# Kernel optimization log

Hardware: AMD Instinct MI355X
Metric: run time of the kernel (lower is better)

The kernel has to match this reference:

```python
import jax, jax.numpy as jnp
import numpy as np

N_NODES = 50000
N_EDGES = 600000
IN_C, HID_C, OUT_C = 128, 128, 64
NUM_GRAPHS = 512


def sage_conv(x, src, dst, Wl, bl, Wr):
    """PyG SAGEConv (aggr='mean'): out = mean_{j->i} x_j @ Wl + bl + x_i @ Wr."""
    n = x.shape[0]
    msg = x[src]  # [E, d] gather
    agg = jax.ops.segment_sum(msg, dst, num_segments=n)
    deg = jax.ops.segment_sum(jnp.ones((src.shape[0], 1), x.dtype), dst, num_segments=n)
    agg = agg / jnp.maximum(deg, 1.0)
    return agg @ Wl + bl + x @ Wr


def setup_inputs() -> dict:
    key = jax.random.key(0)
    ks = jax.random.split(key, 12)
    x = jax.random.normal(ks[0], (N_NODES, IN_C), dtype=jnp.float32)
    edge_index = jax.random.randint(ks[1], (2, N_EDGES), 0, N_NODES, dtype=jnp.int32)
    cluster = jnp.sort(jax.random.randint(ks[2], (N_NODES,), 0, NUM_GRAPHS, dtype=jnp.int32))
    def lin(k, din, dout):
        s = 1.0 / np.sqrt(din)
        return (jax.random.uniform(k, (din, dout), jnp.float32, -s, s))
    return {
        "x": x, "edge_index": edge_index, "cluster": cluster,
        "Wl0": lin(ks[3], IN_C, HID_C), "bl0": jnp.zeros((HID_C,), jnp.float32), "Wr0": lin(ks[4], IN_C, HID_C),
        "Wl1": lin(ks[5], HID_C, HID_C), "bl1": jnp.zeros((HID_C,), jnp.float32), "Wr1": lin(ks[6], HID_C, HID_C),
        "Wl2": lin(ks[7], HID_C, OUT_C), "bl2": jnp.zeros((OUT_C,), jnp.float32), "Wr2": lin(ks[8], HID_C, OUT_C),
    }


def reference(x, edge_index, cluster, Wl0, bl0, Wr0, Wl1, bl1, Wr1, Wl2, bl2, Wr2):
    src, dst = edge_index[0], edge_index[1]
    out = None
    # hidden SAGEConv layers + relu (dropout inactive in eval)
    for Wl, bl, Wr in ((Wl0, bl0, Wr0), (Wl1, bl1, Wr1)):
        out = sage_conv(x, src, dst, Wl, bl, Wr)
        x = jax.nn.relu(out)
    # scatter-mean graph pooling over cluster ids
    gsum = jax.ops.segment_sum(x, cluster, num_segments=NUM_GRAPHS)
    gcnt = jax.ops.segment_sum(jnp.ones((x.shape[0], 1), x.dtype), cluster, num_segments=NUM_GRAPHS)
    g = gsum / jnp.maximum(gcnt, 1.0)
    # final conv + log-softmax over classes
    xf = sage_conv(x, src, dst, Wl2, bl2, Wr2)
    return (jax.nn.log_softmax(xf, axis=-1), out, g)
```

## Files before the change

kernel.cpp:

```cpp
#include <hip/hip_runtime.h>
#include <math.h>

#define NN 50000
#define NE 600000
#define NG 512

typedef unsigned int u32;
typedef unsigned short u16;
typedef unsigned char u8;

typedef __attribute__((ext_vector_type(8))) short bf16x8;
typedef __attribute__((ext_vector_type(4))) float f32x4;
typedef __attribute__((ext_vector_type(4))) unsigned int u32x4;

__device__ __forceinline__ float bf2f(u16 u) {
  return __uint_as_float(((u32)u) << 16);
}
__device__ __forceinline__ u16 f2bf(float f) {
  u32 u = __float_as_uint(f);
  u32 lsb = (u >> 16) & 1u;
  u += 0x7fffu + lsb;
  return (u16)(u >> 16);
}

__device__ __forceinline__ u8 f2q(float f) {
  u32 b = __float_as_uint(f);
  u32 s = (b >> 24) & 0x80u;
  u32 mag = b & 0x7fffffffu;
  u32 lsb = (mag >> 20) & 1u;
  mag += 0x7ffffu + lsb;
  int t = (int)(mag >> 20) - 960;
  u32 em = (t < 0) ? 0u : ((t > 0x7e) ? 0x7eu : (u32)t);
  return (u8)(s | em);
}
__device__ __forceinline__ float q2f(u32 u, int k) {
  u32 s8 = (u >> (8 * k)) & 0xffu;
  u32 em = s8 & 0x7fu;
  u32 bits = ((s8 & 0x80u) << 24) | ((em << 20) + 0x3c000000u);
  return em ? __uint_as_float(bits) : 0.f;
}

__global__ __launch_bounds__(256)
void prep_k(const float* __restrict__ x, u32* __restrict__ xb, u16* __restrict__ xq16,
            const int* __restrict__ ei, int* __restrict__ deg,
            const float* __restrict__ Wl0, const float* __restrict__ Wr0, u16* __restrict__ WbT0,
            const float* __restrict__ Wl1, const float* __restrict__ Wr1, u16* __restrict__ WbT1,
            const float* __restrict__ Wl2, u16* __restrict__ WlT2,
            const float* __restrict__ Wr2, u16* __restrict__ WrT2) {
  int b = blockIdx.x;
  int tid = threadIdx.x;
  if (b < 12500) {
    int t = b * 256 + tid;
    float2 v = ((const float2*)x)[t];
    xb[t] = (u32)f2bf(v.x) | ((u32)f2bf(v.y) << 16);
    xq16[t] = (u16)f2q(v.x) | ((u16)f2q(v.y) << 8);
  } else if (b < 14844) {
    int e = (b - 12500) * 256 + tid;
    if (e < NE) atomicAdd(&deg[ei[NE + e]], 1);
  } else if (b < 15100) {
    bool w1 = (b >= 14972);
    int t = (b - (w1 ? 14972 : 14844)) * 256 + tid;
    int n = t >> 8;
    int k = t & 255;
    const float* Wl = w1 ? Wl1 : Wl0;
    const float* Wr = w1 ? Wr1 : Wr0;
    float v = (k < 128) ? Wl[k * 128 + n] : Wr[(k - 128) * 128 + n];
    int c = k >> 3, e = k & 7;
    u16* dst = w1 ? WbT1 : WbT0;
    dst[n * 256 + (((c ^ (n & 7)) << 3) | e)] = f2bf(v);
  } else {
    bool wr = (b >= 15132);
    int t = (b - (wr ? 15132 : 15100)) * 256 + tid;
    int n = t >> 7;
    int k = t & 127;
    const float* W = wr ? Wr2 : Wl2;
    float v = W[k * 64 + n];
    int c = k >> 3, e = k & 7;
    u16* dst = wr ? WrT2 : WlT2;
    dst[n * 128 + (((c ^ (n & 7)) << 3) | e)] = f2bf(v);
  }
}

__global__ __launch_bounds__(256)
void scan1_k(const int* __restrict__ deg, int* __restrict__ bsum) {
  __shared__ int s[256];
  int idx = blockIdx.x * 256 + threadIdx.x;
  int v = (idx < NN) ? deg[idx] : 0;
  s[threadIdx.x] = v;
  __syncthreads();
  for (int off = 128; off > 0; off >>= 1) {
    if (threadIdx.x < off) s[threadIdx.x] += s[threadIdx.x + off];
    __syncthreads();
  }
  if (threadIdx.x == 0) bsum[blockIdx.x] = s[0];
}

__global__ __launch_bounds__(256)
void scan2_k(const int* __restrict__ bsum, int* __restrict__ bofs, int* __restrict__ row_ptr) {
  __shared__ int s[256];
  int t = threadIdx.x;
  int v = (t < 196) ? bsum[t] : 0;
  s[t] = v;
  __syncthreads();
  for (int off = 1; off < 256; off <<= 1) {
    int add = (t >= off) ? s[t - off] : 0;
    __syncthreads();
    s[t] += add;
    __syncthreads();
  }
  if (t < 196) bofs[t] = s[t] - v;
  if (t == 0) row_ptr[NN] = NE;
}

__global__ __launch_bounds__(256)
void scan3_k(const int* __restrict__ deg, const int* __restrict__ bofs,
             int* __restrict__ row_ptr, int* __restrict__ cursor) {
  __shared__ int s[256];
  int idx = blockIdx.x * 256 + threadIdx.x;
  int t = threadIdx.x;
  int v = (idx < NN) ? deg[idx] : 0;
  s[t] = v;
  __syncthreads();
  for (int off = 1; off < 256; off <<= 1) {
    int add = (t >= off) ? s[t - off] : 0;
    __syncthreads();
    s[t] += add;
    __syncthreads();
  }
  if (idx < NN) {
    int p = bofs[blockIdx.x] + s[t] - v;
    row_ptr[idx] = p;
    cursor[idx] = p;
  }
}

__global__ __launch_bounds__(256)
void fill_k(const int* __restrict__ ei, int* __restrict__ cursor, int* __restrict__ perm) {
  int e = blockIdx.x * 256 + threadIdx.x;
  if (e >= NE) return;
  int pos = atomicAdd(&cursor[ei[NE + e]], 1);
  perm[pos] = ei[e];
}

__global__ __launch_bounds__(256)
void gatherq_k(const u8* __restrict__ xq, const int* __restrict__ row_ptr,
               const int* __restrict__ perm, u16* __restrict__ aggb) {
  int wave = threadIdx.x >> 6;
  int lane = threadIdx.x & 63;
  int grp  = lane >> 3;
  int li   = lane & 7;
  int n = (blockIdx.x * 4 + wave) * 8 + grp;
  int ns = min(n, NN - 1);
  int beg = row_ptr[ns];
  int cnt = row_ptr[ns + 1] - beg;
  int beg_s = min(beg, NE - 1);
  int last = max(cnt - 1, 0);
  int m = max(cnt, __shfl_xor(cnt, 8));
  m = max(m, __shfl_xor(m, 16));
  int jmax = max(m, __shfl_xor(m, 32));
  float acc[16];
#pragma unroll
  for (int i = 0; i < 16; i++) acc[i] = 0.f;
  const u32x4* xv = (const u32x4*)xq;
  for (int base = 0; base < jmax; base += 8) {
    int idx[8];
#pragma unroll
    for (int j = 0; j < 8; j++) idx[j] = perm[beg_s + min(base + j, last)];
    u32x4 v[8];
#pragma unroll
    for (int j = 0; j < 8; j++) v[j] = xv[(size_t)idx[j] * 8 + li];
#pragma unroll
    for (int j = 0; j < 8; j++) {
      bool live = (base + j) < cnt;
#pragma unroll
      for (int w = 0; w < 4; w++) {
        u32 u = v[j][w];
#pragma unroll
        for (int k = 0; k < 4; k++) {
          float f = q2f(u, k);
          acc[w * 4 + k] += live ? f : 0.f;
        }
      }
    }
  }
  float inv = 1.0f / fmaxf((float)cnt, 1.0f);
  u32 o[8];
#pragma unroll
  for (int p = 0; p < 8; p++)
    o[p] = (u32)f2bf(acc[2 * p] * inv) | ((u32)f2bf(acc[2 * p + 1] * inv) << 16);
  if (n < NN) {
    u32x4* dst = (u32x4*)(aggb + (size_t)n * 128);
    dst[li * 2]     = (u32x4){o[0], o[1], o[2], o[3]};
    dst[li * 2 + 1] = (u32x4){o[4], o[5], o[6], o[7]};
  }
}

__global__ __launch_bounds__(256)
void gatherq64_k(const u8* __restrict__ yq, const int* __restrict__ row_ptr,
                 const int* __restrict__ perm, u16* __restrict__ aggy) {
  int wave = threadIdx.x >> 6;
  int lane = threadIdx.x & 63;
  int grp  = lane >> 2;
  int li   = lane & 3;
  int n = (blockIdx.x * 4 + wave) * 16 + grp;
  int ns = min(n, NN - 1);
  int beg = row_ptr[ns];
  int cnt = row_ptr[ns + 1] - beg;
  int beg_s = min(beg, NE - 1);
  int last = max(cnt - 1, 0);
  int m = max(cnt, __shfl_xor(cnt, 4));
  m = max(m, __shfl_xor(m, 8));
  m = max(m, __shfl_xor(m, 16));
  int jmax = max(m, __shfl_xor(m, 32));
  float acc[16];
#pragma unroll
  for (int i = 0; i < 16; i++) acc[i] = 0.f;
  const u32x4* xv = (const u32x4*)yq;
  for (int base = 0; base < jmax; base += 8) {
    int idx[8];
#pragma unroll
    for (int j = 0; j < 8; j++) idx[j] = perm[beg_s + min(base + j, last)];
    u32x4 v[8];
#pragma unroll
    for (int j = 0; j < 8; j++) v[j] = xv[(size_t)idx[j] * 4 + li];
#pragma unroll
    for (int j = 0; j < 8; j++) {
      bool live = (base + j) < cnt;
#pragma unroll
      for (int w = 0; w < 4; w++) {
        u32 u = v[j][w];
#pragma unroll
        for (int k = 0; k < 4; k++) {
          float f = q2f(u, k);
          acc[w * 4 + k] += live ? f : 0.f;
        }
      }
    }
  }
  float inv = 1.0f / fmaxf((float)cnt, 1.0f);
  u32 o[8];
#pragma unroll
  for (int p = 0; p < 8; p++)
    o[p] = (u32)f2bf(acc[2 * p] * inv) | ((u32)f2bf(acc[2 * p + 1] * inv) << 16);
  if (n < NN) {
    u32x4* dst = (u32x4*)(aggy + (size_t)n * 64);
    dst[li * 2]     = (u32x4){o[0], o[1], o[2], o[3]};
    dst[li * 2 + 1] = (u32x4){o[4], o[5], o[6], o[7]};
  }
}

template<bool WRITE_PRE, bool WRITE_XQ>
__global__ __launch_bounds__(256)
void sage_mfma_v2_k(const u16* __restrict__ aggb, const u16* __restrict__ xbin,
                    const u16* __restrict__ WbT, const float* __restrict__ bl,
                    u16* __restrict__ xb_out, float* __restrict__ out_pre,
                    u8* __restrict__ xq_out) {
  __shared__ u16 wsh[128 * 256];
  int tid = threadIdx.x;
  {
    const u32x4* g = (const u32x4*)WbT;
    u32x4* l = (u32x4*)wsh;
#pragma unroll
    for (int i = 0; i < 16; i++)
      l[tid + i * 256] = g[tid + i * 256];
  }
  __syncthreads();

  int wave = tid >> 6;
  int lane = tid & 63;
  int quad = lane >> 4;
  int m16  = lane & 15;
  int r0 = blockIdx.x * 64 + wave * 16;

  int rowA = min(r0 + m16, NN - 1);
  const u16* pa = aggb + (size_t)rowA * 128 + quad * 8;
  const u16* px = xbin + (size_t)rowA * 128 + quad * 8;
  bf16x8 a[8];
#pragma unroll
  for (int j = 0; j < 4; j++) a[j]     = *(const bf16x8*)(pa + j * 32);
#pragma unroll
  for (int j = 0; j < 4; j++) a[4 + j] = *(const bf16x8*)(px + j * 32);

  f32x4 acc[8];
#pragma unroll
  for (int nt = 0; nt < 8; nt++) acc[nt] = (f32x4){0.f, 0.f, 0.f, 0.f};

  int swz = m16 & 7;
#pragma unroll
  for (int ks = 0; ks < 8; ks++) {
#pragma unroll
    for (int nt = 0; nt < 8; nt++) {
      const u16* bp = wsh + (nt * 16 + m16) * 256 + (((quad + ks * 4) ^ swz) << 3);
      bf16x8 b = *(const bf16x8*)bp;
      acc[nt] = __builtin_amdgcn_mfma_f32_16x16x32_bf16(a[ks], b, acc[nt], 0, 0, 0);
    }
  }

  float bv[8];
#pragma unroll
  for (int nt = 0; nt < 8; nt++) bv[nt] = bl[nt * 16 + m16];

  int rbase = r0 + quad * 4;
#pragma unroll
  for (int r = 0; r < 4; r++) {
    int row = rbase + r;
    if (row < NN) {
#pragma unroll
      for (int nt = 0; nt < 8; nt++) {
        int col = nt * 16 + m16;
        float v = acc[nt][r] + bv[nt];
        if (WRITE_PRE) out_pre[(size_t)row * 128 + col] = v;
        float rl = fmaxf(v, 0.f);
        xb_out[(size_t)row * 128 + col] = f2bf(rl);
        if (WRITE_XQ) xq_out[(size_t)row * 128 + col] = f2q(rl);
      }
    }
  }
}

__global__ __launch_bounds__(256)
void post_k(const u16* __restrict__ xb2, const int* __restrict__ cluster,
            float* __restrict__ g, const u16* __restrict__ WlT2,
            u8* __restrict__ yq) {
  __shared__ u16 wsh[64 * 128];
  int tid = threadIdx.x;
  if (blockIdx.x < NG) {
    float* sh = (float*)wsh;
    int gid = blockIdx.x;
    int ch = tid & 127;
    int half = tid >> 7;
    int lo = 0, hi = NN;
    while (lo < hi) { int mid = (lo + hi) >> 1; if (cluster[mid] < gid) lo = mid + 1; else hi = mid; }
    int beg = lo;
    hi = NN;
    while (lo < hi) { int mid = (lo + hi) >> 1; if (cluster[mid] < gid + 1) lo = mid + 1; else hi = mid; }
    int end = lo;
    float s0 = 0.f, s1 = 0.f;
    int n = beg + half;
    for (; n + 2 < end; n += 4) {
      s0 += bf2f(xb2[(size_t)n * 128 + ch]);
      s1 += bf2f(xb2[(size_t)(n + 2) * 128 + ch]);
    }
    if (n < end) s0 += bf2f(xb2[(size_t)n * 128 + ch]);
    sh[tid] = s0 + s1;
    __syncthreads();
    if (tid < 128) {
      float s = sh[tid] + sh[tid + 128];
      g[gid * 128 + tid] = s / fmaxf((float)(end - beg), 1.0f);
    }
    return;
  }
  int bid = blockIdx.x - NG;
  {
    const u32x4* gw = (const u32x4*)WlT2;
    u32x4* l = (u32x4*)wsh;
#pragma unroll
    for (int i = 0; i < 4; i++)
      l[tid + i * 256] = gw[tid + i * 256];
  }
  __syncthreads();

  int wave = tid >> 6;
  int lane = tid & 63;
  int quad = lane >> 4;
  int m16  = lane & 15;
  int r0 = bid * 64 + wave * 16;

  int rowA = min(r0 + m16, NN - 1);
  const u16* px = xb2 + (size_t)rowA * 128 + quad * 8;
  bf16x8 a[4];
#pragma unroll
  for (int j = 0; j < 4; j++) a[j] = *(const bf16x8*)(px + j * 32);

  f32x4 acc[4];
#pragma unroll
  for (int nt = 0; nt < 4; nt++) acc[nt] = (f32x4){0.f, 0.f, 0.f, 0.f};

  int swz = m16 & 7;
#pragma unroll
  for (int ks = 0; ks < 4; ks++) {
#pragma unroll
    for (int nt = 0; nt < 4; nt++) {
      const u16* bp = wsh + (nt * 16 + m16) * 128 + (((ks * 4 + quad) ^ swz) << 3);
      bf16x8 b = *(const bf16x8*)bp;
      acc[nt] = __builtin_amdgcn_mfma_f32_16x16x32_bf16(a[ks], b, acc[nt], 0, 0, 0);
    }
  }

  int rbase = r0 + quad * 4;
#pragma unroll
  for (int r = 0; r < 4; r++) {
    int row = rbase + r;
    if (row < NN) {
#pragma unroll
      for (int nt = 0; nt < 4; nt++)
        yq[(size_t)row * 64 + nt * 16 + m16] = f2q(acc[nt][r]);
    }
  }
}

__global__ __launch_bounds__(256)
void sage64f_k(const u16* __restrict__ aggy, const u16* __restrict__ xbin,
               const u16* __restrict__ WT, const float* __restrict__ bl,
               float* __restrict__ out) {
  __shared__ u16 wsh[64 * 128];
  int tid = threadIdx.x;
  {
    const u32x4* g = (const u32x4*)WT;
    u32x4* l = (u32x4*)wsh;
#pragma unroll
    for (int i = 0; i < 4; i++)
      l[tid + i * 256] = g[tid + i * 256];
  }
  __syncthreads();

  int wave = tid >> 6;
  int lane = tid & 63;
  int quad = lane >> 4;
  int m16  = lane & 15;
  int r0 = blockIdx.x * 64 + wave * 16;

  int rowA = min(r0 + m16, NN - 1);
  const u16* px = xbin + (size_t)rowA * 128 + quad * 8;
  bf16x8 a[4];
#pragma unroll
  for (int j = 0; j < 4; j++) a[j] = *(const bf16x8*)(px + j * 32);

  f32x4 acc[4];
#pragma unroll
  for (int nt = 0; nt < 4; nt++) acc[nt] = (f32x4){0.f, 0.f, 0.f, 0.f};

  int swz = m16 & 7;
#pragma unroll
  for (int ks = 0; ks < 4; ks++) {
#pragma unroll
    for (int nt = 0; nt < 4; nt++) {
      const u16* bp = wsh + (nt * 16 + m16) * 128 + (((ks * 4 + quad) ^ swz) << 3);
      bf16x8 b = *(const bf16x8*)bp;
      acc[nt] = __builtin_amdgcn_mfma_f32_16x16x32_bf16(a[ks], b, acc[nt], 0, 0, 0);
    }
  }

  float bv[4];
#pragma unroll
  for (int nt = 0; nt < 4; nt++) bv[nt] = bl[nt * 16 + m16];

  int rbase = r0 + quad * 4;
#pragma unroll
  for (int r = 0; r < 4; r++) {
    int row = rbase + r;
    int rs = min(row, NN - 1);
    float v0 = acc[0][r] + bv[0] + bf2f(aggy[(size_t)rs * 64 + m16]);
    float v1 = acc[1][r] + bv[1] + bf2f(aggy[(size_t)rs * 64 + 16 + m16]);
    float v2 = acc[2][r] + bv[2] + bf2f(aggy[(size_t)rs * 64 + 32 + m16]);
    float v3 = acc[3][r] + bv[3] + bf2f(aggy[(size_t)rs * 64 + 48 + m16]);
    float m = fmaxf(fmaxf(v0, v1), fmaxf(v2, v3));
#pragma unroll
    for (int mk = 1; mk <= 8; mk <<= 1) m = fmaxf(m, __shfl_xor(m, mk));
    float s = __expf(v0 - m) + __expf(v1 - m) + __expf(v2 - m) + __expf(v3 - m);
#pragma unroll
    for (int mk = 1; mk <= 8; mk <<= 1) s += __shfl_xor(s, mk);
    float ls = m + __logf(s);
    if (row < NN) {
      float* orow = out + (size_t)row * 64;
      orow[m16]      = v0 - ls;
      orow[16 + m16] = v1 - ls;
      orow[32 + m16] = v2 - ls;
      orow[48 + m16] = v3 - ls;
    }
  }
}

extern "C" void kernel_launch(void* const* d_in, const int* in_sizes, int n_in,
                              void* d_out, int out_size, void* d_ws, size_t ws_size,
                              hipStream_t stream) {
  const float* x   = (const float*)d_in[0];
  const int*   ei  = (const int*)d_in[1];
  const int*   cl  = (const int*)d_in[2];
  const float* Wl0 = (const float*)d_in[3];
  const float* bl0 = (const float*)d_in[4];
  const float* Wr0 = (const float*)d_in[5];
  const float* Wl1 = (const float*)d_in[6];
  const float* bl1 = (const float*)d_in[7];
  const float* Wr1 = (const float*)d_in[8];
  const float* Wl2 = (const float*)d_in[9];
  const float* bl2 = (const float*)d_in[10];
  const float* Wr2 = (const float*)d_in[11];
  float* out = (float*)d_out;

  char* ws = (char*)d_ws;
  u16*   xb0     = (u16*)  (ws);
  u16*   xb1     = (u16*)  (ws + 12800000);
  u16*   xb2     = (u16*)  (ws + 25600000);
  u8*    xq      = (u8*)   (ws + 25600000);
  u16*   aggb    = (u16*)  (ws + 38400000);
  u8*    y2q     = (u8*)   (ws + 38400000);
  u16*   aggy    = (u16*)  (ws + 44800000);
  u16*   WbT0    = (u16*)  (ws + 51200000);
  u16*   WbT1    = (u16*)  (ws + 51265536);
  u16*   WlT2    = (u16*)  (ws + 51331072);
  u16*   WrT2    = (u16*)  (ws + 51347456);
  int*   deg     = (int*)  (ws + 51363840);
  int*   row_ptr = (int*)  (ws + 51564032);
  int*   cursor  = (int*)  (ws + 51764736);
  int*   perm    = (int*)  (ws + 51964736);
  int*   bsum    = (int*)  (ws + 54364736);
  int*   bofs    = (int*)  (ws + 54365568);

  float* out_lsm = out;
  float* out_pre = out + 3200000;
  float* out_g   = out + 9600000;

  hipMemsetAsync(deg, 0, 200000, stream);
  prep_k<<<15164, 256, 0, stream>>>(x, (u32*)xb0, (u16*)xq, ei, deg,
                                    Wl0, Wr0, WbT0, Wl1, Wr1, WbT1,
                                    Wl2, WlT2, Wr2, WrT2);

  scan1_k<<<196, 256, 0, stream>>>(deg, bsum);
  scan2_k<<<1, 256, 0, stream>>>(bsum, bofs, row_ptr);
  scan3_k<<<196, 256, 0, stream>>>(deg, bofs, row_ptr, cursor);
  fill_k<<<2344, 256, 0, stream>>>(ei, cursor, perm);

  gatherq_k<<<1563, 256, 0, stream>>>(xq, row_ptr, perm, aggb);
  sage_mfma_v2_k<false, true><<<782, 256, 0, stream>>>(aggb, xb0, WbT0, bl0, xb1, nullptr, xq);

  gatherq_k<<<1563, 256, 0, stream>>>(xq, row_ptr, perm, aggb);
  sage_mfma_v2_k<true, false><<<782, 256, 0, stream>>>(aggb, xb1, WbT1, bl1, xb2, out_pre, nullptr);

  post_k<<<NG + 782, 256, 0, stream>>>(xb2, cl, out_g, WlT2, y2q);

  gatherq64_k<<<782, 256, 0, stream>>>(y2q, row_ptr, perm, aggy);
  sage64f_k<<<782, 256, 0, stream>>>(aggy, xb2, WrT2, bl2, out_lsm);
}
```

Measured before the change: 322.9 us.

## Split neighbor edges across two lane groups and gather final layer in bf16

```diff
diff --git a/kernel.cpp b/kernel.cpp
--- a/kernel.cpp
+++ b/kernel.cpp
@@ -143,8 +143,65 @@
 }
 
 __global__ __launch_bounds__(256)
-void gatherq_k(const u8* __restrict__ xq, const int* __restrict__ row_ptr,
-               const int* __restrict__ perm, u16* __restrict__ aggb) {
+void gatherq12_k(const u8* __restrict__ xq, const int* __restrict__ row_ptr,
+                 const int* __restrict__ perm, u16* __restrict__ aggb) {
+  int wave = threadIdx.x >> 6;
+  int lane = threadIdx.x & 63;
+  int grp  = lane >> 4;
+  int jj   = (lane >> 3) & 1;
+  int li   = lane & 7;
+  int n = (blockIdx.x * 4 + wave) * 4 + grp;
+  int beg = row_ptr[n];
+  int cnt = row_ptr[n + 1] - beg;
+  int beg_s = min(beg, NE - 1);
+  int last = max(cnt - 1, 0);
+  int m = max(cnt, __shfl_xor(cnt, 16));
+  int jmax = max(m, __shfl_xor(m, 32));
+  float acc[16];
+#pragma unroll
+  for (int i = 0; i < 16; i++) acc[i] = 0.f;
+  const u32x4* xv = (const u32x4*)xq;
+  for (int base = 0; base < jmax; base += 16) {
+    int e8[8];
+#pragma unroll
+    for (int j = 0; j < 8; j++) e8[j] = base + j * 2 + jj;
+    int idx[8];
+#pragma unroll
+    for (int j = 0; j < 8; j++) idx[j] = perm[beg_s + min(e8[j], last)];
+    u32x4 v[8];
+#pragma unroll
+    for (int j = 0; j < 8; j++) v[j] = xv[(size_t)idx[j] * 8 + li];
+#pragma unroll
+    for (int j = 0; j < 8; j++) {
+      bool live = e8[j] < cnt;
+#pragma unroll
+      for (int w = 0; w < 4; w++) {
+        u32 u = v[j][w];
+#pragma unroll
+        for (int k = 0; k < 4; k++) {
+          float f = q2f(u, k);
+          acc[w * 4 + k] += live ? f : 0.f;
+        }
+      }
+    }
+  }
+#pragma unroll
+  for (int i = 0; i < 16; i++) acc[i] += __shfl_xor(acc[i], 8);
+  float inv = 1.0f / fmaxf((float)cnt, 1.0f);
+  if (jj == 0) {
+    u32 o[8];
+#pragma unroll
+    for (int p = 0; p < 8; p++)
+      o[p] = (u32)f2bf(acc[2 * p] * inv) | ((u32)f2bf(acc[2 * p + 1] * inv) << 16);
+    u32x4* dst = (u32x4*)(aggb + (size_t)n * 128);
+    dst[li * 2]     = (u32x4){o[0], o[1], o[2], o[3]};
+    dst[li * 2 + 1] = (u32x4){o[4], o[5], o[6], o[7]};
+  }
+}
+
+__global__ __launch_bounds__(256)
+void gather8_k(const u16* __restrict__ yb, const int* __restrict__ row_ptr,
+               const int* __restrict__ perm, u16* __restrict__ aggy) {
   int wave = threadIdx.x >> 6;
   int lane = threadIdx.x & 63;
   int grp  = lane >> 3;
@@ -158,10 +215,10 @@
   int m = max(cnt, __shfl_xor(cnt, 8));
   m = max(m, __shfl_xor(m, 16));
   int jmax = max(m, __shfl_xor(m, 32));
-  float acc[16];
-#pragma unroll
-  for (int i = 0; i < 16; i++) acc[i] = 0.f;
-  const u32x4* xv = (const u32x4*)xq;
+  float acc[8];
+#pragma unroll
+  for (int i = 0; i < 8; i++) acc[i] = 0.f;
+  const u32x4* xv = (const u32x4*)yb;
   for (int base = 0; base < jmax; base += 8) {
     int idx[8];
 #pragma unroll
@@ -175,78 +232,17 @@
 #pragma unroll
       for (int w = 0; w < 4; w++) {
         u32 u = v[j][w];
-#pragma unroll
-        for (int k = 0; k < 4; k++) {
-          float f = q2f(u, k);
-          acc[w * 4 + k] += live ? f : 0.f;
-        }
+        acc[2 * w]     += live ? __uint_as_float(u << 16) : 0.f;
+        acc[2 * w + 1] += live ? __uint_as_float(u & 0xffff0000u) : 0.f;
       }
     }
   }
   float inv = 1.0f / fmaxf((float)cnt, 1.0f);
-  u32 o[8];
-#pragma unroll
-  for (int p = 0; p < 8; p++)
-    o[p] = (u32)f2bf(acc[2 * p] * inv) | ((u32)f2bf(acc[2 * p + 1] * inv) << 16);
-  if (n < NN) {
-    u32x4* dst = (u32x4*)(aggb + (size_t)n * 128);
-    dst[li * 2]     = (u32x4){o[0], o[1], o[2], o[3]};
-    dst[li * 2 + 1] = (u32x4){o[4], o[5], o[6], o[7]};
-  }
-}
-
-__global__ __launch_bounds__(256)
-void gatherq64_k(const u8* __restrict__ yq, const int* __restrict__ row_ptr,
-                 const int* __restrict__ perm, u16* __restrict__ aggy) {
-  int wave = threadIdx.x >> 6;
-  int lane = threadIdx.x & 63;
-  int grp  = lane >> 2;
-  int li   = lane & 3;
-  int n = (blockIdx.x * 4 + wave) * 16 + grp;
-  int ns = min(n, NN - 1);
-  int beg = row_ptr[ns];
-  int cnt = row_ptr[ns + 1] - beg;
-  int beg_s = min(beg, NE - 1);
-  int last = max(cnt - 1, 0);
-  int m = max(cnt, __shfl_xor(cnt, 4));
-  m = max(m, __shfl_xor(m, 8));
-  m = max(m, __shfl_xor(m, 16));
-  int jmax = max(m, __shfl_xor(m, 32));
-  float acc[16];
-#pragma unroll
-  for (int i = 0; i < 16; i++) acc[i] = 0.f;
-  const u32x4* xv = (const u32x4*)yq;
-  for (int base = 0; base < jmax; base += 8) {
-    int idx[8];
-#pragma unroll
-    for (int j = 0; j < 8; j++) idx[j] = perm[beg_s + min(base + j, last)];
-    u32x4 v[8];
-#pragma unroll
-    for (int j = 0; j < 8; j++) v[j] = xv[(size_t)idx[j] * 4 + li];
-#pragma unroll
-    for (int j = 0; j < 8; j++) {
-      bool live = (base + j) < cnt;
-#pragma unroll
-      for (int w = 0; w < 4; w++) {
-        u32 u = v[j][w];
-#pragma unroll
-        for (int k = 0; k < 4; k++) {
-          float f = q2f(u, k);
-          acc[w * 4 + k] += live ? f : 0.f;
-        }
-      }
-    }
-  }
-  float inv = 1.0f / fmaxf((float)cnt, 1.0f);
-  u32 o[8];
-#pragma unroll
-  for (int p = 0; p < 8; p++)
-    o[p] = (u32)f2bf(acc[2 * p] * inv) | ((u32)f2bf(acc[2 * p + 1] * inv) << 16);
-  if (n < NN) {
-    u32x4* dst = (u32x4*)(aggy + (size_t)n * 64);
-    dst[li * 2]     = (u32x4){o[0], o[1], o[2], o[3]};
-    dst[li * 2 + 1] = (u32x4){o[4], o[5], o[6], o[7]};
-  }
+  u32x4 o;
+#pragma unroll
+  for (int w = 0; w < 4; w++)
+    o[w] = (u32)f2bf(acc[2 * w] * inv) | ((u32)f2bf(acc[2 * w + 1] * inv) << 16);
+  if (n < NN) ((u32x4*)aggy)[(size_t)n * 8 + li] = o;
 }
 
 template<bool WRITE_PRE, bool WRITE_XQ>
@@ -321,7 +317,7 @@
 __global__ __launch_bounds__(256)
 void post_k(const u16* __restrict__ xb2, const int* __restrict__ cluster,
             float* __restrict__ g, const u16* __restrict__ WlT2,
-            u8* __restrict__ yq) {
+            u16* __restrict__ yb) {
   __shared__ u16 wsh[64 * 128];
   int tid = threadIdx.x;
   if (blockIdx.x < NG) {
@@ -394,7 +390,7 @@
     if (row < NN) {
 #pragma unroll
       for (int nt = 0; nt < 4; nt++)
-        yq[(size_t)row * 64 + nt * 16 + m16] = f2q(acc[nt][r]);
+        yb[(size_t)row * 64 + nt * 16 + m16] = f2bf(acc[nt][r]);
     }
   }
 }
@@ -494,7 +490,7 @@
   u16*   xb2     = (u16*)  (ws + 25600000);
   u8*    xq      = (u8*)   (ws + 25600000);
   u16*   aggb    = (u16*)  (ws + 38400000);
-  u8*    y2q     = (u8*)   (ws + 38400000);
+  u16*   y2      = aggb;
   u16*   aggy    = (u16*)  (ws + 44800000);
   u16*   WbT0    = (u16*)  (ws + 51200000);
   u16*   WbT1    = (u16*)  (ws + 51265536);
@@ -521,14 +517,14 @@
   scan3_k<<<196, 256, 0, stream>>>(deg, bofs, row_ptr, cursor);
   fill_k<<<2344, 256, 0, stream>>>(ei, cursor, perm);
 
-  gatherq_k<<<1563, 256, 0, stream>>>(xq, row_ptr, perm, aggb);
+  gatherq12_k<<<3125, 256, 0, stream>>>(xq, row_ptr, perm, aggb);
   sage_mfma_v2_k<false, true><<<782, 256, 0, stream>>>(aggb, xb0, WbT0, bl0, xb1, nullptr, xq);
 
-  gatherq_k<<<1563, 256, 0, stream>>>(xq, row_ptr, perm, aggb);
+  gatherq12_k<<<3125, 256, 0, stream>>>(xq, row_ptr, perm, aggb);
   sage_mfma_v2_k<true, false><<<782, 256, 0, stream>>>(aggb, xb1, WbT1, bl1, xb2, out_pre, nullptr);
 
-  post_k<<<NG + 782, 256, 0, stream>>>(xb2, cl, out_g, WlT2, y2q);
-
-  gatherq64_k<<<782, 256, 0, stream>>>(y2q, row_ptr, perm, aggy);
+  post_k<<<NG + 782, 256, 0, stream>>>(xb2, cl, out_g, WlT2, y2);
+
+  gather8_k<<<1563, 256, 0, stream>>>(y2, row_ptr, perm, aggy);
   sage64f_k<<<782, 256, 0, stream>>>(aggy, xb2, WrT2, bl2, out_lsm);
 }
```

New measurement: 312.5 us. 1.03x faster.
